# Performance work log

Hardware: AMD Instinct MI355X
Metric: run time of the kernel (lower is better)

The kernel has to match this reference:

```python
import jax, jax.numpy as jnp
import numpy as np

B, N, FIN, FOUT, K = 8, 1024, 32, 4, 2
FREQS = [2.0, 3.0, 4.0, 5.0]  # q_idx = 1/FREQS[idx]


def setup_inputs() -> dict:
    key = jax.random.key(0)
    k1, k2, k3, k4, k5 = jax.random.split(key, 5)
    X_real = jax.random.normal(k1, (B, N, FIN), jnp.float32)
    X_imag = jax.random.normal(k2, (B, N, FIN), jnp.float32)
    adj = jax.random.uniform(k3, (B, N, N), jnp.float32)  # weighted directed adjacency
    stdv = 1.0 / np.sqrt(FIN)
    weight = jax.random.uniform(k4, (FOUT, K + 1, FIN), jnp.float32, -stdv, stdv)
    bias = jax.random.uniform(k5, (FOUT,), jnp.float32, -stdv, stdv)
    return {"X_real": X_real, "X_imag": X_imag, "adj": adj, "weight": weight, "bias": bias}


def _mag_laplacian(adj, q):
    """Normalized magnetic Laplacian, real/imag parts. adj: [B,N,N]."""
    adj_t = jnp.swapaxes(adj, -1, -2)
    As = 0.5 * (adj + adj_t)                    # symmetrized adjacency
    D = As.sum(-1)                              # degrees [B,N]
    dinv = jnp.where(D > 0, 1.0 / jnp.sqrt(jnp.where(D > 0, D, 1.0)), 0.0)
    theta = (2.0 * np.pi * q) * (adj - adj_t)   # phase matrix
    S = dinv[:, :, None] * As * dinv[:, None, :]  # D^-1/2 As D^-1/2
    I = jnp.eye(N, dtype=adj.dtype)
    L_real = I - S * jnp.cos(theta)
    L_imag = -S * jnp.sin(theta)
    return L_real, L_imag


def _cmatvec(Lr, Li, zr, zi):
    """Complex batched matmul (Lr+iLi) @ (zr+izi); L:[B,N,N], z:[B,N,F]."""
    return Lr @ zr - Li @ zi, Li @ zr + Lr @ zi


def reference(X_real, X_imag, adj, weight, bias):
    outs_r, outs_i = [], []
    for idx in range(FOUT):  # small fixed loop over output channels / frequencies
        q = 1.0 / FREQS[idx]
        Lr, Li = _mag_laplacian(adj, q)
        # Chebyshev polynomials applied directly to the signal:
        # T0 = I -> z0 = X ; T1 = I - L -> z1 = X - L X ; T_k = 2 L T_{k-1} + T_{k-2}
        z = [(X_real, X_imag)]
        hr, hi = _cmatvec(Lr, Li, X_real, X_imag)
        z.append((X_real - hr, X_imag - hi))
        for i in range(2, K + 1):
            mr, mi = _cmatvec(Lr, Li, z[i - 1][0], z[i - 1][1])
            z.append((2.0 * mr + z[i - 2][0], 2.0 * mi + z[i - 2][1]))
        Zr = jnp.stack([t[0] for t in z], 0)  # [K+1, B, N, FIN]
        Zi = jnp.stack([t[1] for t in z], 0)
        or_ = jnp.einsum('kbnf,kf->bn', Zr, weight[idx]) + bias[idx]
        oi_ = jnp.einsum('kbnf,kf->bn', Zi, weight[idx])
        outs_r.append(or_)
        outs_i.append(oi_)
    return jnp.stack(outs_r, -1), jnp.stack(outs_i, -1)  # each [B, N, FOUT]
```

## Files before the change

### kernel.cpp

```cpp
#include <hip/hip_runtime.h>
#include <cstddef>

#define NB 8
#define NN 1024
#define NF 32
#define NIDX 4
#define JC 4
#define JCH 256
#define NJT 4
#define TIB 32

#define OFF_ROW   0u
#define OFF_COLP  8192u
#define OFF_DINV  532480u
#define OFF_P     540672u
#define OFF_R     606208u
#define OFF_WT    671744u
#define OFF_WP    737280u

#if __has_builtin(__builtin_amdgcn_sinf)
#define FSIN(x) __builtin_amdgcn_sinf(x)
#define FCOS(x) __builtin_amdgcn_cosf(x)
#else
#define FSIN(x) __sinf((x) * 6.283185307179586f)
#define FCOS(x) __cosf((x) * 6.283185307179586f)
#endif

__global__ __launch_bounds__(512) void k_sums(const float* __restrict__ adj,
                                              float* __restrict__ rowsum,
                                              float* __restrict__ colpart) {
  int b = blockIdx.x, strip = blockIdx.y;
  int t = threadIdx.x, lane = t & 63, w = t >> 6;
  float colreg[16];
  #pragma unroll
  for (int i = 0; i < 16; ++i) colreg[i] = 0.f;
  int r0 = strip*16 + w*2;
  #pragma unroll
  for (int rr = 0; rr < 2; ++rr) {
    const float4* row4 = reinterpret_cast<const float4*>(adj + ((size_t)b*NN + r0 + rr)*NN);
    float rs = 0.f;
    #pragma unroll
    for (int cq = 0; cq < 4; ++cq) {
      float4 v = row4[cq*64 + lane];
      colreg[cq*4+0] += v.x; colreg[cq*4+1] += v.y;
      colreg[cq*4+2] += v.z; colreg[cq*4+3] += v.w;
      rs += (v.x + v.y) + (v.z + v.w);
    }
    #pragma unroll
    for (int o = 32; o > 0; o >>= 1) rs += __shfl_xor(rs, o);
    if (lane == 0) rowsum[b*NN + r0 + rr] = rs;
  }
  __shared__ float cacc[8][NN];
  #pragma unroll
  for (int cq = 0; cq < 4; ++cq)
    #pragma unroll
    for (int x = 0; x < 4; ++x) cacc[w][cq*256 + lane*4 + x] = colreg[cq*4+x];
  __syncthreads();
  for (int c = t; c < NN; c += 512) {
    float s = 0.f;
    #pragma unroll
    for (int ww = 0; ww < 8; ++ww) s += cacc[ww][c];
    colpart[(size_t)strip*(NB*NN) + b*NN + c] = s;
  }
}

__global__ __launch_bounds__(256) void k_prep(const float* __restrict__ Xr, const float* __restrict__ Xi,
                       const float* __restrict__ weight,
                       const float* __restrict__ rowsum, const float* __restrict__ colpart,
                       const float* __restrict__ bias,
                       float* __restrict__ dinv,
                       float* __restrict__ pvec, float* __restrict__ rvec,
                       float* __restrict__ out) {
  __shared__ float wsm[NIDX*3*NF];
  int t = threadIdx.x;
  for (int e = t; e < NIDX*3*NF; e += 256) wsm[e] = weight[e];
  __syncthreads();
  int gid = blockIdx.x*256 + t;
  float cs = 0.f;
  for (int k = 0; k < 64; ++k) cs += colpart[(size_t)k*(NB*NN) + gid];
  float D = 0.5f*(rowsum[gid] + cs);
  float di = (D > 0.f) ? (1.0f / sqrtf(D)) : 0.f;
  dinv[gid] = di;
  const float* xr = Xr + (size_t)gid*NF;
  const float* xi = Xi + (size_t)gid*NF;
  float acc[NIDX][3][2];
  #pragma unroll
  for (int x = 0; x < NIDX; ++x)
    #pragma unroll
    for (int v = 0; v < 3; ++v) { acc[x][v][0] = 0.f; acc[x][v][1] = 0.f; }
  for (int f = 0; f < NF; ++f) {
    float xrf = xr[f], xif = xi[f];
    #pragma unroll
    for (int x = 0; x < NIDX; ++x) {
      float w0 = wsm[x*96 + f], w1 = wsm[x*96 + 32 + f], w2 = wsm[x*96 + 64 + f];
      float av = w0 + w2, bv = w1 + 2.f*w2, cv = -2.f*w2;
      acc[x][0][0] += av*xrf; acc[x][0][1] += av*xif;
      acc[x][1][0] += bv*xrf; acc[x][1][1] += bv*xif;
      acc[x][2][0] += cv*xrf; acc[x][2][1] += cv*xif;
    }
  }
  #pragma unroll
  for (int x = 0; x < NIDX; ++x) {
    size_t o = (size_t)gid*8 + x*2;
    pvec[o] = acc[x][1][0];      pvec[o+1] = acc[x][1][1];
    rvec[o] = di*acc[x][2][0];   rvec[o+1] = di*acc[x][2][1];
    out[gid*4 + x]         = acc[x][0][0] + bias[x];
    out[32768 + gid*4 + x] = acc[x][0][1];
  }
}

__global__ void k_mid(const float* __restrict__ dinv, const float* __restrict__ pvec,
                      const float* __restrict__ wpart, float* __restrict__ wtot) {
  int o = blockIdx.x*256 + threadIdx.x;
  float v = pvec[o];
  #pragma unroll
  for (int c = 0; c < JC; ++c) v += wpart[(size_t)c*65536 + o];
  wtot[o] = v * dinv[o >> 3];
}

template<int MODE>
__global__ __launch_bounds__(256, 4) void k_pass(const float* __restrict__ adj,
                                                 const float* __restrict__ dinv,
                                                 const float* __restrict__ vin,
                                                 float* __restrict__ outp) {
  __shared__ float Tjs[64][33];
  __shared__ float red[4][8*72];
  int b = blockIdx.x, i0 = blockIdx.y*TIB, zc = blockIdx.z;
  int t = threadIdx.x, lane = t & 63, w = t >> 6;
  int wu = __builtin_amdgcn_readfirstlane(w);
  int ibase = i0 + wu*8;
  float accr[8][NIDX], acci[8][NIDX];
  #pragma unroll
  for (int s = 0; s < 8; ++s)
    #pragma unroll
    for (int x = 0; x < NIDX; ++x) { accr[s][x] = 0.f; acci[s][x] = 0.f; }

  for (int jt = 0; jt < NJT; ++jt) {
    int j0 = zc*JCH + jt*64;
    __syncthreads();
    #pragma unroll
    for (int m = 0; m < 2; ++m) {
      int e4 = t + 256*m;
      int jj = e4 >> 3, i4 = (e4 & 7) << 2;
      float4 vv = *reinterpret_cast<const float4*>(adj + ((size_t)b*NN + j0 + jj)*NN + i0 + i4);
      float* dst = &Tjs[jj][i4];
      dst[0] = vv.x; dst[1] = vv.y; dst[2] = vv.z; dst[3] = vv.w;
    }
    int jg = j0 + lane;
    const float4* vp = reinterpret_cast<const float4*>(vin + ((size_t)b*NN + jg)*8);
    float4 v0 = vp[0], v1 = vp[1];
    float vr[NIDX] = {v0.x, v0.z, v1.x, v1.z};
    float vi[NIDX] = {v0.y, v0.w, v1.y, v1.w};
    __syncthreads();
    const float* arb = adj + ((size_t)b*NN + ibase)*NN + j0 + lane;
    #pragma unroll
    for (int s = 0; s < 8; ++s) {
      float ar = arb[(size_t)s*NN];
      float ac = Tjs[lane][wu*8 + s];
      float dd = ar - ac, sm = ar + ac;
      float s4 = FSIN(0.25f*dd), c4 = FCOS(0.25f*dd);
      float s3 = FSIN((1.f/3.f)*dd), c3 = FCOS((1.f/3.f)*dd);
      float s5 = FSIN(0.2f*dd), c5 = FCOS(0.2f*dd);
      float c2 = 1.f - 2.f*s4*s4, s2 = 2.f*s4*c4;
      float csv[NIDX] = {c2, c3, c4, c5};
      float snv[NIDX] = {s2, s3, s4, s5};
      #pragma unroll
      for (int x = 0; x < NIDX; ++x) {
        float A = sm*csv[x], B = sm*snv[x];
        accr[s][x] += A*vr[x] - B*vi[x];
        acci[s][x] += A*vi[x] + B*vr[x];
      }
    }
  }

  bool b1 = (lane & 1), b2 = (lane & 2), b4 = (lane & 4);
  #pragma unroll
  for (int s = 0; s < 8; ++s) {
    float v0 = accr[s][0], v1 = acci[s][0], v2 = accr[s][1], v3 = acci[s][1];
    float v4 = accr[s][2], v5 = acci[s][2], v6 = accr[s][3], v7 = acci[s][3];
    float k0 = b1 ? v1 : v0, s0 = b1 ? v0 : v1;
    float k1 = b1 ? v3 : v2, s1 = b1 ? v2 : v3;
    float k2 = b1 ? v5 : v4, s2 = b1 ? v4 : v5;
    float k3 = b1 ? v7 : v6, s3 = b1 ? v6 : v7;
    v0 = k0 + __shfl_xor(s0, 1);
    v1 = k1 + __shfl_xor(s1, 1);
    v2 = k2 + __shfl_xor(s2, 1);
    v3 = k3 + __shfl_xor(s3, 1);
    k0 = b2 ? v1 : v0; s0 = b2 ? v0 : v1;
    k1 = b2 ? v3 : v2; s1 = b2 ? v2 : v3;
    v0 = k0 + __shfl_xor(s0, 2);
    v1 = k1 + __shfl_xor(s1, 2);
    k0 = b4 ? v1 : v0; s0 = b4 ? v0 : v1;
    v0 = k0 + __shfl_xor(s0, 4);
    red[w][s*72 + (lane & 7)*9 + (lane >> 3)] = v0;
  }
  __syncthreads();
  {
    int row = lane >> 3, slot = lane & 7;
    float sum = 0.f;
    #pragma unroll
    for (int g = 0; g < 8; ++g) sum += red[w][row*72 + slot*9 + g];
    int gi = b*NN + ibase + row;
    float val = sum * 0.5f * dinv[gi];
    if constexpr (MODE == 0) outp[(size_t)zc*65536 + (size_t)gi*8 + slot] = val;
    else atomicAdd(&outp[(slot & 1)*32768 + gi*4 + (slot >> 1)], val);
  }
}

extern "C" void kernel_launch(void* const* d_in, const int* in_sizes, int n_in,
                              void* d_out, int out_size, void* d_ws, size_t ws_size,
                              hipStream_t stream) {
  (void)in_sizes; (void)n_in; (void)out_size; (void)ws_size;
  const float* Xr     = (const float*)d_in[0];
  const float* Xi     = (const float*)d_in[1];
  const float* adj    = (const float*)d_in[2];
  const float* weight = (const float*)d_in[3];
  const float* bias   = (const float*)d_in[4];
  float* ws = (float*)d_ws;
  float* rowsum  = ws + OFF_ROW;
  float* colpart = ws + OFF_COLP;
  float* dinv    = ws + OFF_DINV;
  float* pvec    = ws + OFF_P;
  float* rvec    = ws + OFF_R;
  float* wtot    = ws + OFF_WT;
  float* wpart   = ws + OFF_WP;
  float* out = (float*)d_out;

  k_sums<<<dim3(NB, 64), 512, 0, stream>>>(adj, rowsum, colpart);
  k_prep<<<dim3(NB*NN/256), 256, 0, stream>>>(Xr, Xi, weight, rowsum, colpart, bias,
                                              dinv, pvec, rvec, out);
  k_pass<0><<<dim3(NB, NN/TIB, JC), 256, 0, stream>>>(adj, dinv, rvec, wpart);
  k_mid<<<dim3(256), 256, 0, stream>>>(dinv, pvec, wpart, wtot);
  k_pass<1><<<dim3(NB, NN/TIB, JC), 256, 0, stream>>>(adj, dinv, wtot, out);
}
```

Baseline: 55.15 us.

## Exploit Hermitian symmetry of magnetic Laplacian to process only upper-triangle tiles

The pass kernels now iterate over 136 upper-triangular 64x64 tile pairs instead of the full matrix. Each tile's sin/cos phase evaluation is reused for both L·v on the i-rows and the conjugate-transpose contribution on the j-rows, roughly halving transcendental work and adjacency reads. Partial results are accumulated with atomics into a zero-initialised buffer rather than written as per-chunk partials. The cost is more atomic traffic, extra registers for the j accumulators, and fewer blocks (8x136 versus 8x128 with larger per-block work), which may hurt occupancy or load balance.

```diff
diff --git a/kernel.cpp b/kernel.cpp
--- a/kernel.cpp
+++ b/kernel.cpp
@@ -5,10 +5,8 @@
 #define NN 1024
 #define NF 32
 #define NIDX 4
-#define JC 4
-#define JCH 256
-#define NJT 4
-#define TIB 32
+#define NTILE 16
+#define NPAIR 136
 
 #define OFF_ROW   0u
 #define OFF_COLP  8192u
@@ -70,7 +68,7 @@
                        const float* __restrict__ bias,
                        float* __restrict__ dinv,
                        float* __restrict__ pvec, float* __restrict__ rvec,
-                       float* __restrict__ out) {
+                       float* __restrict__ wpart, float* __restrict__ out) {
   __shared__ float wsm[NIDX*3*NF];
   int t = threadIdx.x;
   for (int e = t; e < NIDX*3*NF; e += 256) wsm[e] = weight[e];
@@ -104,6 +102,7 @@
     size_t o = (size_t)gid*8 + x*2;
     pvec[o] = acc[x][1][0];      pvec[o+1] = acc[x][1][1];
     rvec[o] = di*acc[x][2][0];   rvec[o+1] = di*acc[x][2][1];
+    wpart[o] = 0.f;              wpart[o+1] = 0.f;
     out[gid*4 + x]         = acc[x][0][0] + bias[x];
     out[32768 + gid*4 + x] = acc[x][0][1];
   }
@@ -112,98 +111,127 @@
 __global__ void k_mid(const float* __restrict__ dinv, const float* __restrict__ pvec,
                       const float* __restrict__ wpart, float* __restrict__ wtot) {
   int o = blockIdx.x*256 + threadIdx.x;
-  float v = pvec[o];
-  #pragma unroll
-  for (int c = 0; c < JC; ++c) v += wpart[(size_t)c*65536 + o];
-  wtot[o] = v * dinv[o >> 3];
+  wtot[o] = (pvec[o] + wpart[o]) * dinv[o >> 3];
 }
 
 template<int MODE>
-__global__ __launch_bounds__(256, 4) void k_pass(const float* __restrict__ adj,
-                                                 const float* __restrict__ dinv,
-                                                 const float* __restrict__ vin,
-                                                 float* __restrict__ outp) {
-  __shared__ float Tjs[64][33];
-  __shared__ float red[4][8*72];
-  int b = blockIdx.x, i0 = blockIdx.y*TIB, zc = blockIdx.z;
+__global__ __launch_bounds__(256, 4) void k_hpass(const float* __restrict__ adj,
+                                                  const float* __restrict__ dinv,
+                                                  const float* __restrict__ vin,
+                                                  float* __restrict__ outacc) {
+  __shared__ float Tjs[64][65];
+  __shared__ float vil[64][8];
+  __shared__ float red[4][576];
+  int b = blockIdx.x;
+  int pid = blockIdx.y;
+  int ti = 0, rem = pid;
+  while (rem >= NTILE - ti) { rem -= NTILE - ti; ++ti; }
+  int tj = ti + rem;
+  bool diag = (ti == tj);
+  int i0 = ti*64, j0 = tj*64;
   int t = threadIdx.x, lane = t & 63, w = t >> 6;
   int wu = __builtin_amdgcn_readfirstlane(w);
-  int ibase = i0 + wu*8;
-  float accr[8][NIDX], acci[8][NIDX];
-  #pragma unroll
-  for (int s = 0; s < 8; ++s)
-    #pragma unroll
-    for (int x = 0; x < NIDX; ++x) { accr[s][x] = 0.f; acci[s][x] = 0.f; }
-
-  for (int jt = 0; jt < NJT; ++jt) {
-    int j0 = zc*JCH + jt*64;
-    __syncthreads();
-    #pragma unroll
-    for (int m = 0; m < 2; ++m) {
-      int e4 = t + 256*m;
-      int jj = e4 >> 3, i4 = (e4 & 7) << 2;
-      float4 vv = *reinterpret_cast<const float4*>(adj + ((size_t)b*NN + j0 + jj)*NN + i0 + i4);
-      float* dst = &Tjs[jj][i4];
-      dst[0] = vv.x; dst[1] = vv.y; dst[2] = vv.z; dst[3] = vv.w;
-    }
-    int jg = j0 + lane;
-    const float4* vp = reinterpret_cast<const float4*>(vin + ((size_t)b*NN + jg)*8);
-    float4 v0 = vp[0], v1 = vp[1];
-    float vr[NIDX] = {v0.x, v0.z, v1.x, v1.z};
-    float vi[NIDX] = {v0.y, v0.w, v1.y, v1.w};
-    __syncthreads();
+
+  #pragma unroll
+  for (int m = 0; m < 4; ++m) {
+    int e4 = t + 256*m;
+    int jj = e4 >> 4, i4 = (e4 & 15) << 2;
+    float4 vv = *reinterpret_cast<const float4*>(adj + ((size_t)b*NN + j0 + jj)*NN + i0 + i4);
+    float* dst = &Tjs[jj][i4];
+    dst[0] = vv.x; dst[1] = vv.y; dst[2] = vv.z; dst[3] = vv.w;
+  }
+  for (int e = t; e < 64*8; e += 256)
+    vil[e >> 3][e & 7] = vin[((size_t)b*NN + i0 + (e >> 3))*8 + (e & 7)];
+  const float4* vb = reinterpret_cast<const float4*>(vin + ((size_t)b*NN + j0 + lane)*8);
+  float4 a4 = vb[0], c4 = vb[1];
+  float vrj[NIDX] = {a4.x, a4.z, c4.x, c4.z};
+  float vij[NIDX] = {a4.y, a4.w, c4.y, c4.w};
+  __syncthreads();
+
+  float jar[NIDX] = {0.f,0.f,0.f,0.f}, jai[NIDX] = {0.f,0.f,0.f,0.f};
+  bool b1 = (lane & 1), b2 = (lane & 2), b4 = (lane & 4);
+
+  #pragma unroll
+  for (int step = 0; step < 2; ++step) {
+    int ibase = i0 + step*32 + wu*8;
+    float accr[8][NIDX], acci[8][NIDX];
+    #pragma unroll
+    for (int s = 0; s < 8; ++s)
+      #pragma unroll
+      for (int x = 0; x < NIDX; ++x) { accr[s][x] = 0.f; acci[s][x] = 0.f; }
     const float* arb = adj + ((size_t)b*NN + ibase)*NN + j0 + lane;
     #pragma unroll
     for (int s = 0; s < 8; ++s) {
       float ar = arb[(size_t)s*NN];
-      float ac = Tjs[lane][wu*8 + s];
+      float ac = Tjs[lane][step*32 + wu*8 + s];
       float dd = ar - ac, sm = ar + ac;
-      float s4 = FSIN(0.25f*dd), c4 = FCOS(0.25f*dd);
+      float s4 = FSIN(0.25f*dd), c4w = FCOS(0.25f*dd);
       float s3 = FSIN((1.f/3.f)*dd), c3 = FCOS((1.f/3.f)*dd);
       float s5 = FSIN(0.2f*dd), c5 = FCOS(0.2f*dd);
-      float c2 = 1.f - 2.f*s4*s4, s2 = 2.f*s4*c4;
-      float csv[NIDX] = {c2, c3, c4, c5};
+      float c2 = 1.f - 2.f*s4*s4, s2 = 2.f*s4*c4w;
+      float csv[NIDX] = {c2, c3, c4w, c5};
       float snv[NIDX] = {s2, s3, s4, s5};
+      const float* vi8 = &vil[step*32 + wu*8 + s][0];
       #pragma unroll
       for (int x = 0; x < NIDX; ++x) {
         float A = sm*csv[x], B = sm*snv[x];
-        accr[s][x] += A*vr[x] - B*vi[x];
-        acci[s][x] += A*vi[x] + B*vr[x];
+        accr[s][x] += A*vrj[x] - B*vij[x];
+        acci[s][x] += A*vij[x] + B*vrj[x];
+        if (!diag) {
+          float vri = vi8[x*2], vii = vi8[x*2 + 1];
+          jar[x] += A*vri + B*vii;
+          jai[x] += A*vii - B*vri;
+        }
       }
     }
-  }
-
-  bool b1 = (lane & 1), b2 = (lane & 2), b4 = (lane & 4);
-  #pragma unroll
-  for (int s = 0; s < 8; ++s) {
-    float v0 = accr[s][0], v1 = acci[s][0], v2 = accr[s][1], v3 = acci[s][1];
-    float v4 = accr[s][2], v5 = acci[s][2], v6 = accr[s][3], v7 = acci[s][3];
-    float k0 = b1 ? v1 : v0, s0 = b1 ? v0 : v1;
-    float k1 = b1 ? v3 : v2, s1 = b1 ? v2 : v3;
-    float k2 = b1 ? v5 : v4, s2 = b1 ? v4 : v5;
-    float k3 = b1 ? v7 : v6, s3 = b1 ? v6 : v7;
-    v0 = k0 + __shfl_xor(s0, 1);
-    v1 = k1 + __shfl_xor(s1, 1);
-    v2 = k2 + __shfl_xor(s2, 1);
-    v3 = k3 + __shfl_xor(s3, 1);
-    k0 = b2 ? v1 : v0; s0 = b2 ? v0 : v1;
-    k1 = b2 ? v3 : v2; s1 = b2 ? v2 : v3;
-    v0 = k0 + __shfl_xor(s0, 2);
-    v1 = k1 + __shfl_xor(s1, 2);
-    k0 = b4 ? v1 : v0; s0 = b4 ? v0 : v1;
-    v0 = k0 + __shfl_xor(s0, 4);
-    red[w][s*72 + (lane & 7)*9 + (lane >> 3)] = v0;
-  }
-  __syncthreads();
-  {
-    int row = lane >> 3, slot = lane & 7;
-    float sum = 0.f;
-    #pragma unroll
-    for (int g = 0; g < 8; ++g) sum += red[w][row*72 + slot*9 + g];
-    int gi = b*NN + ibase + row;
-    float val = sum * 0.5f * dinv[gi];
-    if constexpr (MODE == 0) outp[(size_t)zc*65536 + (size_t)gi*8 + slot] = val;
-    else atomicAdd(&outp[(slot & 1)*32768 + gi*4 + (slot >> 1)], val);
+    #pragma unroll
+    for (int s = 0; s < 8; ++s) {
+      float v0 = accr[s][0], v1 = acci[s][0], v2 = accr[s][1], v3 = acci[s][1];
+      float v4 = accr[s][2], v5 = acci[s][2], v6 = accr[s][3], v7 = acci[s][3];
+      float k0 = b1 ? v1 : v0, s0 = b1 ? v0 : v1;
+      float k1 = b1 ? v3 : v2, s1 = b1 ? v2 : v3;
+      float k2 = b1 ? v5 : v4, s2 = b1 ? v4 : v5;
+      float k3 = b1 ? v7 : v6, s3 = b1 ? v6 : v7;
+      v0 = k0 + __shfl_xor(s0, 1);
+      v1 = k1 + __shfl_xor(s1, 1);
+      v2 = k2 + __shfl_xor(s2, 1);
+      v3 = k3 + __shfl_xor(s3, 1);
+      k0 = b2 ? v1 : v0; s0 = b2 ? v0 : v1;
+      k1 = b2 ? v3 : v2; s1 = b2 ? v2 : v3;
+      v0 = k0 + __shfl_xor(s0, 2);
+      v1 = k1 + __shfl_xor(s1, 2);
+      k0 = b4 ? v1 : v0; s0 = b4 ? v0 : v1;
+      v0 = k0 + __shfl_xor(s0, 4);
+      red[w][s*72 + (lane & 7)*9 + (lane >> 3)] = v0;
+    }
+    {
+      int row = lane >> 3, slot = lane & 7;
+      float sum = 0.f;
+      #pragma unroll
+      for (int g = 0; g < 8; ++g) sum += red[w][row*72 + slot*9 + g];
+      int gi = b*NN + ibase + row;
+      float val = sum * 0.5f * dinv[gi];
+      if constexpr (MODE == 0) atomicAdd(&outacc[(size_t)gi*8 + slot], val);
+      else atomicAdd(&outacc[(slot & 1)*32768 + gi*4 + (slot >> 1)], val);
+    }
+  }
+
+  if (!diag) {
+    __syncthreads();
+    #pragma unroll
+    for (int x = 0; x < NIDX; ++x) {
+      red[w][lane*9 + x*2]     = jar[x];
+      red[w][lane*9 + x*2 + 1] = jai[x];
+    }
+    __syncthreads();
+    for (int e = t; e < 64*8; e += 256) {
+      int jl = e >> 3, slot = e & 7;
+      float sum = red[0][jl*9+slot] + red[1][jl*9+slot] + red[2][jl*9+slot] + red[3][jl*9+slot];
+      int gj = b*NN + j0 + jl;
+      float val = sum * 0.5f * dinv[gj];
+      if constexpr (MODE == 0) atomicAdd(&outacc[(size_t)gj*8 + slot], val);
+      else atomicAdd(&outacc[(slot & 1)*32768 + gj*4 + (slot >> 1)], val);
+    }
   }
 }
 
@@ -228,8 +256,8 @@
 
   k_sums<<<dim3(NB, 64), 512, 0, stream>>>(adj, rowsum, colpart);
   k_prep<<<dim3(NB*NN/256), 256, 0, stream>>>(Xr, Xi, weight, rowsum, colpart, bias,
-                                              dinv, pvec, rvec, out);
-  k_pass<0><<<dim3(NB, NN/TIB, JC), 256, 0, stream>>>(adj, dinv, rvec, wpart);
+                                              dinv, pvec, rvec, wpart, out);
+  k_hpass<0><<<dim3(NB, NPAIR), 256, 0, stream>>>(adj, dinv, rvec, wpart);
   k_mid<<<dim3(256), 256, 0, stream>>>(dinv, pvec, wpart, wtot);
-  k_pass<1><<<dim3(NB, NN/TIB, JC), 256, 0, stream>>>(adj, dinv, wtot, out);
-}
+  k_hpass<1><<<dim3(NB, NPAIR), 256, 0, stream>>>(adj, dinv, wtot, out);
+}
```

After: 73.26 us. +32.8%, slower.

## Cache symmetric/antisymmetric adjacency as fp16 pairs for second pass, drop mid kernel

Applied to the files above, without the earlier changes.

The first Chebyshev pass now writes (adj+adjT, adj-adjT) packed as half2 into a workspace array, so the second pass reads one 4-byte word per element instead of a row read plus a transposed tile gather from the fp32 adjacency. Partial sums from the first pass are accumulated with atomics directly into the pre-seeded wtot buffer, which removes the intermediate k_mid kernel. The first pass also uses 512-thread blocks with 64-row tiles. The fp16 storage lowers precision of the phase and magnitude terms, and the first pass now has an extra full-size store.

```diff
diff --git a/kernel.cpp b/kernel.cpp
--- a/kernel.cpp
+++ b/kernel.cpp
@@ -1,4 +1,5 @@
 #include <hip/hip_runtime.h>
+#include <hip/hip_fp16.h>
 #include <cstddef>
 
 #define NB 8
@@ -6,17 +7,13 @@
 #define NF 32
 #define NIDX 4
 #define JC 4
-#define JCH 256
-#define NJT 4
-#define TIB 32
 
 #define OFF_ROW   0u
 #define OFF_COLP  8192u
 #define OFF_DINV  532480u
-#define OFF_P     540672u
-#define OFF_R     606208u
-#define OFF_WT    671744u
-#define OFF_WP    737280u
+#define OFF_R     540672u
+#define OFF_WT    606208u
+#define OFF_SMDD  671744u
 
 #if __has_builtin(__builtin_amdgcn_sinf)
 #define FSIN(x) __builtin_amdgcn_sinf(x)
@@ -26,6 +23,36 @@
 #define FCOS(x) __cosf((x) * 6.283185307179586f)
 #endif
 
+#define TRIG6(dd, csv, snv)                                          \
+  float s4 = FSIN(0.25f*(dd)), c4w = FCOS(0.25f*(dd));               \
+  float s3 = FSIN((1.f/3.f)*(dd)), c3 = FCOS((1.f/3.f)*(dd));        \
+  float s5 = FSIN(0.2f*(dd)), c5 = FCOS(0.2f*(dd));                  \
+  float c2 = 1.f - 2.f*s4*s4, s2 = 2.f*s4*c4w;                       \
+  csv[0]=c2; csv[1]=c3; csv[2]=c4w; csv[3]=c5;                       \
+  snv[0]=s2; snv[1]=s3; snv[2]=s4; snv[3]=s5;
+
+#define TREDUCE(accr, acci, red, w, lane, b1, b2, b4)                \
+  _Pragma("unroll")                                                  \
+  for (int s = 0; s < 8; ++s) {                                      \
+    float v0 = accr[s][0], v1 = acci[s][0], v2 = accr[s][1], v3 = acci[s][1]; \
+    float v4 = accr[s][2], v5 = acci[s][2], v6 = accr[s][3], v7 = acci[s][3]; \
+    float k0 = b1 ? v1 : v0, s0 = b1 ? v0 : v1;                      \
+    float k1 = b1 ? v3 : v2, s1 = b1 ? v2 : v3;                      \
+    float k2 = b1 ? v5 : v4, s2_ = b1 ? v4 : v5;                     \
+    float k3 = b1 ? v7 : v6, s3_ = b1 ? v6 : v7;                     \
+    v0 = k0 + __shfl_xor(s0, 1);                                     \
+    v1 = k1 + __shfl_xor(s1, 1);                                     \
+    v2 = k2 + __shfl_xor(s2_, 1);                                    \
+    v3 = k3 + __shfl_xor(s3_, 1);                                    \
+    k0 = b2 ? v1 : v0; s0 = b2 ? v0 : v1;                            \
+    k1 = b2 ? v3 : v2; s1 = b2 ? v2 : v3;                            \
+    v0 = k0 + __shfl_xor(s0, 2);                                     \
+    v1 = k1 + __shfl_xor(s1, 2);                                     \
+    k0 = b4 ? v1 : v0; s0 = b4 ? v0 : v1;                            \
+    v0 = k0 + __shfl_xor(s0, 4);                                     \
+    red[w][s*72 + (lane & 7)*9 + (lane >> 3)] = v0;                  \
+  }
+
 __global__ __launch_bounds__(512) void k_sums(const float* __restrict__ adj,
                                               float* __restrict__ rowsum,
                                               float* __restrict__ colpart) {
@@ -68,9 +95,8 @@
                        const float* __restrict__ weight,
                        const float* __restrict__ rowsum, const float* __restrict__ colpart,
                        const float* __restrict__ bias,
-                       float* __restrict__ dinv,
-                       float* __restrict__ pvec, float* __restrict__ rvec,
-                       float* __restrict__ out) {
+                       float* __restrict__ dinv, float* __restrict__ rvec,
+                       float* __restrict__ wtot, float* __restrict__ out) {
   __shared__ float wsm[NIDX*3*NF];
   int t = threadIdx.x;
   for (int e = t; e < NIDX*3*NF; e += 256) wsm[e] = weight[e];
@@ -102,68 +128,58 @@
   #pragma unroll
   for (int x = 0; x < NIDX; ++x) {
     size_t o = (size_t)gid*8 + x*2;
-    pvec[o] = acc[x][1][0];      pvec[o+1] = acc[x][1][1];
     rvec[o] = di*acc[x][2][0];   rvec[o+1] = di*acc[x][2][1];
+    wtot[o] = acc[x][1][0];      wtot[o+1] = acc[x][1][1];
     out[gid*4 + x]         = acc[x][0][0] + bias[x];
     out[32768 + gid*4 + x] = acc[x][0][1];
   }
 }
 
-__global__ void k_mid(const float* __restrict__ dinv, const float* __restrict__ pvec,
-                      const float* __restrict__ wpart, float* __restrict__ wtot) {
-  int o = blockIdx.x*256 + threadIdx.x;
-  float v = pvec[o];
-  #pragma unroll
-  for (int c = 0; c < JC; ++c) v += wpart[(size_t)c*65536 + o];
-  wtot[o] = v * dinv[o >> 3];
-}
-
-template<int MODE>
-__global__ __launch_bounds__(256, 4) void k_pass(const float* __restrict__ adj,
-                                                 const float* __restrict__ dinv,
-                                                 const float* __restrict__ vin,
-                                                 float* __restrict__ outp) {
-  __shared__ float Tjs[64][33];
-  __shared__ float red[4][8*72];
-  int b = blockIdx.x, i0 = blockIdx.y*TIB, zc = blockIdx.z;
-  int t = threadIdx.x, lane = t & 63, w = t >> 6;
+__global__ __launch_bounds__(512, 4) void k_pass0(const float* __restrict__ adj,
+                                                  const float* __restrict__ dinv,
+                                                  const float* __restrict__ rvec,
+                                                  unsigned* __restrict__ smdd,
+                                                  float* __restrict__ wtot) {
+  __shared__ float Tjs[64][65];
+  __shared__ float red[8][8*72];
+  int b = blockIdx.x, i0 = blockIdx.y*64, zc = blockIdx.z;
+  int j0base = zc*(NN/JC);
+  int t = threadIdx.x, lane = t & 63;
+  int w = t >> 6;
   int wu = __builtin_amdgcn_readfirstlane(w);
-  int ibase = i0 + wu*8;
+
   float accr[8][NIDX], acci[8][NIDX];
   #pragma unroll
   for (int s = 0; s < 8; ++s)
     #pragma unroll
     for (int x = 0; x < NIDX; ++x) { accr[s][x] = 0.f; acci[s][x] = 0.f; }
 
-  for (int jt = 0; jt < NJT; ++jt) {
-    int j0 = zc*JCH + jt*64;
+  for (int jt = 0; jt < (NN/JC)/64; ++jt) {
+    int j0 = j0base + jt*64;
     __syncthreads();
     #pragma unroll
     for (int m = 0; m < 2; ++m) {
-      int e4 = t + 256*m;
-      int jj = e4 >> 3, i4 = (e4 & 7) << 2;
+      int e4 = t + 512*m;
+      int jj = e4 >> 4, i4 = (e4 & 15) << 2;
       float4 vv = *reinterpret_cast<const float4*>(adj + ((size_t)b*NN + j0 + jj)*NN + i0 + i4);
       float* dst = &Tjs[jj][i4];
       dst[0] = vv.x; dst[1] = vv.y; dst[2] = vv.z; dst[3] = vv.w;
     }
-    int jg = j0 + lane;
-    const float4* vp = reinterpret_cast<const float4*>(vin + ((size_t)b*NN + jg)*8);
-    float4 v0 = vp[0], v1 = vp[1];
-    float vr[NIDX] = {v0.x, v0.z, v1.x, v1.z};
-    float vi[NIDX] = {v0.y, v0.w, v1.y, v1.w};
+    const float4* vb = reinterpret_cast<const float4*>(rvec + ((size_t)b*NN + j0 + lane)*8);
+    float4 a = vb[0], c = vb[1];
+    float vr[NIDX] = {a.x, a.z, c.x, c.z};
+    float vi[NIDX] = {a.y, a.w, c.y, c.w};
     __syncthreads();
-    const float* arb = adj + ((size_t)b*NN + ibase)*NN + j0 + lane;
+    const float* arbase = adj + ((size_t)b*NN + i0 + wu*8)*NN + j0 + lane;
     #pragma unroll
     for (int s = 0; s < 8; ++s) {
-      float ar = arb[(size_t)s*NN];
+      float ar = arbase[(size_t)s*NN];
       float ac = Tjs[lane][wu*8 + s];
       float dd = ar - ac, sm = ar + ac;
-      float s4 = FSIN(0.25f*dd), c4 = FCOS(0.25f*dd);
-      float s3 = FSIN((1.f/3.f)*dd), c3 = FCOS((1.f/3.f)*dd);
-      float s5 = FSIN(0.2f*dd), c5 = FCOS(0.2f*dd);
-      float c2 = 1.f - 2.f*s4*s4, s2 = 2.f*s4*c4;
-      float csv[NIDX] = {c2, c3, c4, c5};
-      float snv[NIDX] = {s2, s3, s4, s5};
+      __half2 h = __floats2half2_rn(sm, dd);
+      smdd[((size_t)b*NN + i0 + wu*8 + s)*NN + j0 + lane] = *reinterpret_cast<unsigned*>(&h);
+      float csv[NIDX], snv[NIDX];
+      TRIG6(dd, csv, snv)
       #pragma unroll
       for (int x = 0; x < NIDX; ++x) {
         float A = sm*csv[x], B = sm*snv[x];
@@ -172,28 +188,60 @@
       }
     }
   }
-
   bool b1 = (lane & 1), b2 = (lane & 2), b4 = (lane & 4);
-  #pragma unroll
-  for (int s = 0; s < 8; ++s) {
-    float v0 = accr[s][0], v1 = acci[s][0], v2 = accr[s][1], v3 = acci[s][1];
-    float v4 = accr[s][2], v5 = acci[s][2], v6 = accr[s][3], v7 = acci[s][3];
-    float k0 = b1 ? v1 : v0, s0 = b1 ? v0 : v1;
-    float k1 = b1 ? v3 : v2, s1 = b1 ? v2 : v3;
-    float k2 = b1 ? v5 : v4, s2 = b1 ? v4 : v5;
-    float k3 = b1 ? v7 : v6, s3 = b1 ? v6 : v7;
-    v0 = k0 + __shfl_xor(s0, 1);
-    v1 = k1 + __shfl_xor(s1, 1);
-    v2 = k2 + __shfl_xor(s2, 1);
-    v3 = k3 + __shfl_xor(s3, 1);
-    k0 = b2 ? v1 : v0; s0 = b2 ? v0 : v1;
-    k1 = b2 ? v3 : v2; s1 = b2 ? v2 : v3;
-    v0 = k0 + __shfl_xor(s0, 2);
-    v1 = k1 + __shfl_xor(s1, 2);
-    k0 = b4 ? v1 : v0; s0 = b4 ? v0 : v1;
-    v0 = k0 + __shfl_xor(s0, 4);
-    red[w][s*72 + (lane & 7)*9 + (lane >> 3)] = v0;
-  }
+  TREDUCE(accr, acci, red, w, lane, b1, b2, b4)
+  __syncthreads();
+  {
+    int iloc = w*8 + (lane >> 3), slot = lane & 7;
+    float sum = 0.f;
+    #pragma unroll
+    for (int g = 0; g < 8; ++g) sum += red[w][(lane >> 3)*72 + slot*9 + g];
+    int gi = b*NN + i0 + iloc;
+    atomicAdd(&wtot[(size_t)gi*8 + slot], sum * 0.5f * dinv[gi]);
+  }
+}
+
+__global__ __launch_bounds__(256, 4) void k_pass1(const unsigned* __restrict__ smdd,
+                                                  const float* __restrict__ dinv,
+                                                  const float* __restrict__ wtot,
+                                                  float* __restrict__ out) {
+  __shared__ float red[4][8*72];
+  int b = blockIdx.x, i0 = blockIdx.y*32, zc = blockIdx.z;
+  int t = threadIdx.x, lane = t & 63, w = t >> 6;
+  int wu = __builtin_amdgcn_readfirstlane(w);
+  int ibase = i0 + wu*8;
+  float accr[8][NIDX], acci[8][NIDX];
+  #pragma unroll
+  for (int s = 0; s < 8; ++s)
+    #pragma unroll
+    for (int x = 0; x < NIDX; ++x) { accr[s][x] = 0.f; acci[s][x] = 0.f; }
+
+  for (int jt = 0; jt < (NN/JC)/64; ++jt) {
+    int jg = zc*(NN/JC) + jt*64 + lane;
+    float dj = dinv[b*NN + jg];
+    const float4* vp = reinterpret_cast<const float4*>(wtot + ((size_t)b*NN + jg)*8);
+    float4 va = vp[0], vb = vp[1];
+    float vr[NIDX] = {dj*va.x, dj*va.z, dj*vb.x, dj*vb.z};
+    float vi[NIDX] = {dj*va.y, dj*va.w, dj*vb.y, dj*vb.w};
+    const unsigned* sp = smdd + ((size_t)b*NN + ibase)*NN + jg;
+    #pragma unroll
+    for (int s = 0; s < 8; ++s) {
+      unsigned wrd = sp[(size_t)s*NN];
+      __half2 h = *reinterpret_cast<__half2*>(&wrd);
+      float sm = __low2float(h), dd = __high2float(h);
+      float csv[NIDX], snv[NIDX];
+      TRIG6(dd, csv, snv)
+      #pragma unroll
+      for (int x = 0; x < NIDX; ++x) {
+        float A = sm*csv[x], B = sm*snv[x];
+        accr[s][x] += A*vr[x] - B*vi[x];
+        acci[s][x] += A*vi[x] + B*vr[x];
+      }
+    }
+  }
+
+  bool b1 = (lane & 1), b2 = (lane & 2), b4 = (lane & 4);
+  TREDUCE(accr, acci, red, w, lane, b1, b2, b4)
   __syncthreads();
   {
     int row = lane >> 3, slot = lane & 7;
@@ -202,8 +250,7 @@
     for (int g = 0; g < 8; ++g) sum += red[w][row*72 + slot*9 + g];
     int gi = b*NN + ibase + row;
     float val = sum * 0.5f * dinv[gi];
-    if constexpr (MODE == 0) outp[(size_t)zc*65536 + (size_t)gi*8 + slot] = val;
-    else atomicAdd(&outp[(slot & 1)*32768 + gi*4 + (slot >> 1)], val);
+    atomicAdd(&out[(slot & 1)*32768 + gi*4 + (slot >> 1)], val);
   }
 }
 
@@ -220,16 +267,14 @@
   float* rowsum  = ws + OFF_ROW;
   float* colpart = ws + OFF_COLP;
   float* dinv    = ws + OFF_DINV;
-  float* pvec    = ws + OFF_P;
   float* rvec    = ws + OFF_R;
   float* wtot    = ws + OFF_WT;
-  float* wpart   = ws + OFF_WP;
+  unsigned* smdd = (unsigned*)(ws + OFF_SMDD);
   float* out = (float*)d_out;
 
   k_sums<<<dim3(NB, 64), 512, 0, stream>>>(adj, rowsum, colpart);
   k_prep<<<dim3(NB*NN/256), 256, 0, stream>>>(Xr, Xi, weight, rowsum, colpart, bias,
-                                              dinv, pvec, rvec, out);
-  k_pass<0><<<dim3(NB, NN/TIB, JC), 256, 0, stream>>>(adj, dinv, rvec, wpart);
-  k_mid<<<dim3(256), 256, 0, stream>>>(dinv, pvec, wpart, wtot);
-  k_pass<1><<<dim3(NB, NN/TIB, JC), 256, 0, stream>>>(adj, dinv, wtot, out);
-}
+                                              dinv, rvec, wtot, out);
+  k_pass0<<<dim3(NB, NN/64, JC), 512, 0, stream>>>(adj, dinv, rvec, smdd, wtot);
+  k_pass1<<<dim3(NB, NN/32, JC), 256, 0, stream>>>(smdd, dinv, wtot, out);
+}
```

After: 58.17 us. 5.5% more time.
